# Optimization experiments

Hardware: AMD Instinct MI355X
Metric: run time of the kernel (lower is better)

Reference implementation:

```python
import jax, jax.numpy as jnp
import numpy as np

P = 3          # graph partitions
CO = 64        # out_channels
KS = 9         # temporal kernel size (Gamma)
STRIDE = 1     # temporal stride
EPS = 1e-3     # keras BatchNormalization default epsilon


def setup_inputs() -> dict:
    key = jax.random.key(0)
    k1, k2, k3 = jax.random.split(key, 3)
    x = jax.random.normal(k1, (32, 64, 300, 25), dtype=jnp.float32)      # (N, C_in, L, V)
    A = jax.random.uniform(k2, (3, 25, 25), dtype=jnp.float32)           # (P, V, V)
    W = jax.random.normal(k3, (64, 192), dtype=jnp.float32) * 0.05       # (C_in, C_out*P)
    gamma = jnp.ones((64,), dtype=jnp.float32)
    beta = jnp.zeros((64,), dtype=jnp.float32)
    mean = jnp.zeros((64,), dtype=jnp.float32)
    var = jnp.ones((64,), dtype=jnp.float32)
    return {"x": x, "A": A, "W": W, "gamma": gamma, "beta": beta, "mean": mean, "var": var}


def _lt_matrix(L):
    # sum of shifted identities: lt[r, r + i*STRIDE] = 1 for i in [0, KS//STRIDE)
    lt = jnp.zeros((L, L), dtype=jnp.float32)
    for i in range(KS // STRIDE):
        lt = lt + jnp.eye(L, k=i * STRIDE, dtype=jnp.float32)
    return lt


def reference(x, A, W, gamma, beta, mean, var):
    N, C, L, V = x.shape
    res = x  # identity residual (in_channels == out_channels, stride == 1)
    # 1x1 conv: (N,C,L,V) x (C, CO*P) -> (N, CO*P, L, V); channel k = c*P + p (split into CO groups of P)
    y = jnp.einsum('nclv,ck->nklv', x, W)
    y = y.reshape(N, CO, P, L, V)  # (N, C_out, P, L, V)
    # partitioned graph matmul over joints: contract V with A[p]
    z = jnp.einsum('ncplv,pvw->ncplw', y, A)
    # temporal aggregation via handcrafted banded matrix, then sum over partitions
    lt = _lt_matrix(L)
    t = jnp.einsum('ncplv,lm->ncmv', z, lt)  # partition sum fused into einsum
    # BN (inference) over channel axis + ReLU
    inv = gamma / jnp.sqrt(var + EPS)
    xn = (t - mean[None, :, None, None]) * inv[None, :, None, None] + beta[None, :, None, None]
    xn = jax.nn.relu(xn)
    # residual add + final ReLU (dropout is identity at inference)
    return jax.nn.relu(xn + res)
```

## Files before the change

kernel.cpp:

```cpp
#include <hip/hip_runtime.h>
#include <cstdint>
#include <cstddef>

typedef short bf16x8 __attribute__((ext_vector_type(8)));
typedef float f32x4 __attribute__((ext_vector_type(4)));

#define EPS 1e-3f

__device__ __forceinline__ short f32_to_bf16s(float f) {
    union { float f; uint32_t u; } v; v.f = f;
    uint32_t u = v.u;
    return (short)((u + 0x7FFFu + ((u >> 16) & 1u)) >> 16);
}

__global__ __launch_bounds__(256) void prep_kernel(const float* __restrict__ A,
                                                   const float* __restrict__ W,
                                                   unsigned short* __restrict__ wt,
                                                   unsigned short* __restrict__ at) {
    int idx = blockIdx.x * 256 + threadIdx.x;
    if (idx < 12288) {
        int kp = idx >> 6, ci = idx & 63;
        wt[idx] = (unsigned short)f32_to_bf16s(W[ci * 192 + kp]);
    } else {
        int j = idx - 12288;
        if (j < 3072) {
            int w = j / 96, k = j - w * 96;
            float val = 0.f;
            if (w < 25 && k < 75) {
                int p = k / 25, v = k - p * 25;
                val = A[(p * 25 + v) * 25 + w];
            }
            at[j] = (unsigned short)f32_to_bf16s(val);
        }
    }
}

__global__ __launch_bounds__(512, 4) void mega_kernel(
    const float* __restrict__ x,
    const unsigned short* __restrict__ wt,
    const unsigned short* __restrict__ at,
    const float* __restrict__ gamma, const float* __restrict__ beta,
    const float* __restrict__ mean, const float* __restrict__ var,
    float* __restrict__ out) {
    int ch = blockIdx.x, n = blockIdx.y;
    int l0 = ch * 10;
    int tid = threadIdx.x;
    int wv = tid >> 6, lane = tid & 63, q = lane >> 4, lcol = lane & 15;

    __shared__ short smem[16640];
    __shared__ float scs[64], shs[64];

    if (tid < 64) {
        float sc = gamma[tid] * rsqrtf(var[tid] + EPS);
        scs[tid] = sc;
        shs[tid] = beta[tid] - mean[tid] * sc;
    }

    #pragma unroll 1
    for (int rep = 0; rep < 4; ++rep) {
        int cidx = tid + rep * 512;
        if (cidx < 1600) {
            int ci = cidx / 25, v = cidx - ci * 25;
            const float* xp = x + (size_t)(n * 64 + ci) * 7500 + v;
            float vals[18];
            #pragma unroll
            for (int i = 0; i < 18; ++i) {
                int l = l0 - 8 + i;
                vals[i] = (l >= 0) ? xp[l * 25] : 0.f;
            }
            float run = 0.f;
            #pragma unroll
            for (int i = 0; i < 8; ++i) run += vals[i];
            int base = (ci >> 3) * 2056 + (ci & 7);
            #pragma unroll
            for (int j = 0; j < 10; ++j) {
                run += vals[j + 8];
                smem[base + (j * 25 + v) * 8] = f32_to_bf16s(run);
                run -= vals[j];
            }
        }
    }
    __syncthreads();

    bf16x8 b1[2][2];
    #pragma unroll
    for (int nt = 0; nt < 2; ++nt)
        #pragma unroll
        for (int s = 0; s < 2; ++s) {
            int col = wv * 32 + nt * 16 + lcol;
            b1[nt][s] = *(const bf16x8*)&smem[(4 * s + q) * 2056 + col * 8];
        }
    bf16x8 b2[2][3];
    #pragma unroll
    for (int nt = 0; nt < 2; ++nt)
        #pragma unroll
        for (int s = 0; s < 3; ++s)
            b2[nt][s] = *(const bf16x8*)(at + (size_t)(nt * 16 + lcol) * 96 + 32 * s + 8 * q);
    __syncthreads();

    for (int i = tid; i < 5120; i += 512) {
        int r = i >> 5, jj = 72 + (i & 31);
        smem[r * 104 + jj] = 0;
    }

    for (int g = 0; g < 4; ++g) {
        f32x4 acc[3][2];
        #pragma unroll
        for (int mt = 0; mt < 3; ++mt)
            #pragma unroll
            for (int nt = 0; nt < 2; ++nt) acc[mt][nt] = (f32x4){0.f, 0.f, 0.f, 0.f};
        #pragma unroll
        for (int s = 0; s < 2; ++s)
            #pragma unroll
            for (int mt = 0; mt < 3; ++mt) {
                bf16x8 a1 = *(const bf16x8*)(wt + (size_t)(g * 48 + mt * 16 + lcol) * 64 + 32 * s + 8 * q);
                #pragma unroll
                for (int nt = 0; nt < 2; ++nt)
                    acc[mt][nt] = __builtin_amdgcn_mfma_f32_16x16x32_bf16(a1, b1[nt][s], acc[mt][nt], 0, 0, 0);
            }
        __syncthreads();
        #pragma unroll
        for (int mt = 0; mt < 3; ++mt)
            #pragma unroll
            for (int nt = 0; nt < 2; ++nt) {
                int col = wv * 32 + nt * 16 + lcol;
                if (col < 250) {
                    int ll = col / 25, v = col - ll * 25;
                    #pragma unroll
                    for (int r = 0; r < 4; ++r) {
                        int kp = mt * 16 + 4 * q + r;
                        int cl = kp / 3, p = kp - cl * 3;
                        smem[(ll * 16 + cl) * 104 + p * 25 + v] = f32_to_bf16s(acc[mt][nt][r]);
                    }
                }
            }
        __syncthreads();
        for (int l = wv; l < 10; l += 8) {
            f32x4 c0 = {0.f, 0.f, 0.f, 0.f}, c1 = {0.f, 0.f, 0.f, 0.f};
            #pragma unroll
            for (int s = 0; s < 3; ++s) {
                bf16x8 a2 = *(const bf16x8*)&smem[(l * 16 + lcol) * 104 + 32 * s + 8 * q];
                c0 = __builtin_amdgcn_mfma_f32_16x16x32_bf16(a2, b2[0][s], c0, 0, 0, 0);
                c1 = __builtin_amdgcn_mfma_f32_16x16x32_bf16(a2, b2[1][s], c1, 0, 0, 0);
            }
            #pragma unroll
            for (int nt = 0; nt < 2; ++nt) {
                int w = nt * 16 + lcol;
                if (w < 25) {
                    f32x4 cc = nt ? c1 : c0;
                    #pragma unroll
                    for (int r = 0; r < 4; ++r) {
                        int c = g * 16 + 4 * q + r;
                        size_t gi = ((size_t)(n * 64 + c) * 300 + (l0 + l)) * 25 + w;
                        float o = fmaxf(cc[r] * scs[c] + shs[c], 0.f);
                        out[gi] = fmaxf(o + x[gi], 0.f);
                    }
                }
            }
        }
    }
}

extern "C" void kernel_launch(void* const* d_in, const int* in_sizes, int n_in,
                              void* d_out, int out_size, void* d_ws, size_t ws_size,
                              hipStream_t stream) {
    const float* x     = (const float*)d_in[0];
    const float* A     = (const float*)d_in[1];
    const float* W     = (const float*)d_in[2];
    const float* gamma = (const float*)d_in[3];
    const float* beta  = (const float*)d_in[4];
    const float* mean  = (const float*)d_in[5];
    const float* var   = (const float*)d_in[6];
    float* out = (float*)d_out;

    char* ws = (char*)d_ws;
    unsigned short* wt = (unsigned short*)ws;
    unsigned short* at = (unsigned short*)(ws + 24576);

    prep_kernel<<<60, 256, 0, stream>>>(A, W, wt, at);
    mega_kernel<<<dim3(30, 32), 512, 0, stream>>>(x, wt, at, gamma, beta, mean, var, out);
}
```

Before: 167.4 us.

## Batch x loads, prefetch residual early, rebalance graph-MFMA tiles across all waves

```diff
diff --git a/kernel.cpp b/kernel.cpp
--- a/kernel.cpp
+++ b/kernel.cpp
@@ -56,27 +56,53 @@
         shs[tid] = beta[tid] - mean[tid] * sc;
     }
 
-    #pragma unroll 1
-    for (int rep = 0; rep < 4; ++rep) {
-        int cidx = tid + rep * 512;
-        if (cidx < 1600) {
+    {
+        float va[3][18];
+        #pragma unroll
+        for (int rep = 0; rep < 3; ++rep) {
+            int cidx = tid + rep * 512;
             int ci = cidx / 25, v = cidx - ci * 25;
             const float* xp = x + (size_t)(n * 64 + ci) * 7500 + v;
-            float vals[18];
             #pragma unroll
             for (int i = 0; i < 18; ++i) {
                 int l = l0 - 8 + i;
-                vals[i] = (l >= 0) ? xp[l * 25] : 0.f;
-            }
+                va[rep][i] = (l >= 0) ? xp[l * 25] : 0.f;
+            }
+        }
+        #pragma unroll
+        for (int rep = 0; rep < 3; ++rep) {
+            int cidx = tid + rep * 512;
+            int ci = cidx / 25, v = cidx - ci * 25;
             float run = 0.f;
             #pragma unroll
-            for (int i = 0; i < 8; ++i) run += vals[i];
+            for (int i = 0; i < 8; ++i) run += va[rep][i];
             int base = (ci >> 3) * 2056 + (ci & 7);
             #pragma unroll
             for (int j = 0; j < 10; ++j) {
-                run += vals[j + 8];
+                run += va[rep][j + 8];
                 smem[base + (j * 25 + v) * 8] = f32_to_bf16s(run);
-                run -= vals[j];
+                run -= va[rep][j];
+            }
+        }
+        if (tid < 64) {
+            int cidx = 1536 + tid;
+            int ci = cidx / 25, v = cidx - ci * 25;
+            const float* xp = x + (size_t)(n * 64 + ci) * 7500 + v;
+            float vt[18];
+            #pragma unroll
+            for (int i = 0; i < 18; ++i) {
+                int l = l0 - 8 + i;
+                vt[i] = (l >= 0) ? xp[l * 25] : 0.f;
+            }
+            float run = 0.f;
+            #pragma unroll
+            for (int i = 0; i < 8; ++i) run += vt[i];
+            int base = (ci >> 3) * 2056 + (ci & 7);
+            #pragma unroll
+            for (int j = 0; j < 10; ++j) {
+                run += vt[j + 8];
+                smem[base + (j * 25 + v) * 8] = f32_to_bf16s(run);
+                run -= vt[j];
             }
         }
     }
@@ -118,6 +144,23 @@
                 for (int nt = 0; nt < 2; ++nt)
                     acc[mt][nt] = __builtin_amdgcn_mfma_f32_16x16x32_bf16(a1, b1[nt][s], acc[mt][nt], 0, 0, 0);
             }
+
+        float xres[3][4];
+        size_t gbase[3];
+        #pragma unroll
+        for (int t = 0; t < 3; ++t) {
+            int j = wv + 8 * t;
+            int l = j >> 1, nt = j & 1;
+            int w = nt * 16 + lcol;
+            bool valid = (j < 20) && (w < 25);
+            int c0 = g * 16 + 4 * q;
+            size_t gi0 = ((size_t)(n * 64 + c0) * 300 + (l0 + l)) * 25 + w;
+            gbase[t] = gi0;
+            #pragma unroll
+            for (int r = 0; r < 4; ++r)
+                xres[t][r] = valid ? x[gi0 + (size_t)r * 7500] : 0.f;
+        }
+
         __syncthreads();
         #pragma unroll
         for (int mt = 0; mt < 3; ++mt)
@@ -135,25 +178,26 @@
                 }
             }
         __syncthreads();
-        for (int l = wv; l < 10; l += 8) {
-            f32x4 c0 = {0.f, 0.f, 0.f, 0.f}, c1 = {0.f, 0.f, 0.f, 0.f};
-            #pragma unroll
-            for (int s = 0; s < 3; ++s) {
-                bf16x8 a2 = *(const bf16x8*)&smem[(l * 16 + lcol) * 104 + 32 * s + 8 * q];
-                c0 = __builtin_amdgcn_mfma_f32_16x16x32_bf16(a2, b2[0][s], c0, 0, 0, 0);
-                c1 = __builtin_amdgcn_mfma_f32_16x16x32_bf16(a2, b2[1][s], c1, 0, 0, 0);
-            }
-            #pragma unroll
-            for (int nt = 0; nt < 2; ++nt) {
+
+        #pragma unroll
+        for (int t = 0; t < 3; ++t) {
+            int j = wv + 8 * t;
+            if (j < 20) {
+                int l = j >> 1, nt = j & 1;
                 int w = nt * 16 + lcol;
+                f32x4 cacc = {0.f, 0.f, 0.f, 0.f};
+                #pragma unroll
+                for (int s = 0; s < 3; ++s) {
+                    bf16x8 a2 = *(const bf16x8*)&smem[(l * 16 + lcol) * 104 + 32 * s + 8 * q];
+                    cacc = __builtin_amdgcn_mfma_f32_16x16x32_bf16(a2, b2[nt][s], cacc, 0, 0, 0);
+                }
                 if (w < 25) {
-                    f32x4 cc = nt ? c1 : c0;
                     #pragma unroll
                     for (int r = 0; r < 4; ++r) {
                         int c = g * 16 + 4 * q + r;
-                        size_t gi = ((size_t)(n * 64 + c) * 300 + (l0 + l)) * 25 + w;
-                        float o = fmaxf(cc[r] * scs[c] + shs[c], 0.f);
-                        out[gi] = fmaxf(o + x[gi], 0.f);
+                        float o = fmaxf(cacc[r] * scs[c] + shs[c], 0.f);
+                        float res = fmaxf(o + xres[t][r], 0.f);
+                        __builtin_nontemporal_store(res, &out[gbase[t] + (size_t)r * 7500]);
                     }
                 }
             }
```

New measurement: 172.6 us. 3.1% more time.

## Stage x tile in LDS with float4 loads and reuse it for residual

Applied to the files above, without the earlier changes.

```diff
diff --git a/kernel.cpp b/kernel.cpp
--- a/kernel.cpp
+++ b/kernel.cpp
@@ -9,8 +9,11 @@
 
 __device__ __forceinline__ short f32_to_bf16s(float f) {
     union { float f; uint32_t u; } v; v.f = f;
-    uint32_t u = v.u;
-    return (short)((u + 0x7FFFu + ((u >> 16) & 1u)) >> 16);
+    return (short)((v.u + 0x7FFFu + ((v.u >> 16) & 1u)) >> 16);
+}
+__device__ __forceinline__ float bf16s_to_f32(short s) {
+    union { uint32_t u; float f; } v; v.u = ((uint32_t)(unsigned short)s) << 16;
+    return v.f;
 }
 
 __global__ __launch_bounds__(256) void prep_kernel(const float* __restrict__ A,
@@ -42,107 +45,179 @@
     const float* __restrict__ gamma, const float* __restrict__ beta,
     const float* __restrict__ mean, const float* __restrict__ var,
     float* __restrict__ out) {
-    int ch = blockIdx.x, n = blockIdx.y;
-    int l0 = ch * 10;
-    int tid = threadIdx.x;
-    int wv = tid >> 6, lane = tid & 63, q = lane >> 4, lcol = lane & 15;
-
-    __shared__ short smem[16640];
+    const int ch = blockIdx.x, n = blockIdx.y;
+    const int l0 = ch * 8;
+    const int tid = threadIdx.x;
+    const int wv = tid >> 6, lane = tid & 63, q = lane >> 4, lcol = lane & 15;
+
+    __shared__ __align__(16) short R0[13312];
+    __shared__ __align__(16) short XsB[13312];
     __shared__ float scs[64], shs[64];
 
+    bf16x8 b2[2][3];
+    #pragma unroll
+    for (int nt = 0; nt < 2; ++nt)
+        #pragma unroll
+        for (int s = 0; s < 3; ++s)
+            b2[nt][s] = *(const bf16x8*)(at + (size_t)(nt * 16 + lcol) * 96 + 32 * s + 8 * q);
     if (tid < 64) {
         float sc = gamma[tid] * rsqrtf(var[tid] + EPS);
         scs[tid] = sc;
         shs[tid] = beta[tid] - mean[tid] * sc;
     }
 
+    {
+        const float* xn = x + (size_t)n * 480000;
+        const int e0 = l0 * 25 - 200;
+        #pragma unroll
+        for (int rep = 0; rep < 13; ++rep) {
+            int i = tid + rep * 512;
+            if (i < 6400) {
+                int ci = i / 100, j = i - ci * 100;
+                int eg = e0 + 4 * j;
+                float4 val = make_float4(0.f, 0.f, 0.f, 0.f);
+                if (eg >= 0 && eg <= 7496)
+                    val = *(const float4*)(xn + (size_t)ci * 7500 + eg);
+                short4 sv;
+                sv.x = f32_to_bf16s(val.x); sv.y = f32_to_bf16s(val.y);
+                sv.z = f32_to_bf16s(val.z); sv.w = f32_to_bf16s(val.w);
+                if (j < 50) *(short4*)&R0[ci * 208 + 4 * j] = sv;
+                else        *(short4*)&XsB[ci * 208 + 4 * (j - 50)] = sv;
+            }
+        }
+    }
+    __syncthreads();
+
+    float hv[4][8];
+    #pragma unroll
+    for (int rep = 0; rep < 3; ++rep) {
+        int col = tid + rep * 512;
+        int ci = col / 25, v = col - ci * 25;
+        const short* hp = &R0[ci * 208 + v];
+        #pragma unroll
+        for (int m = 0; m < 8; ++m) hv[rep][m] = bf16s_to_f32(hp[m * 25]);
+    }
+    if (tid < 64) {
+        int col = 1536 + tid;
+        int ci = col / 25, v = col - ci * 25;
+        const short* hp = &R0[ci * 208 + v];
+        #pragma unroll
+        for (int m = 0; m < 8; ++m) hv[3][m] = bf16s_to_f32(hp[m * 25]);
+    }
+    __syncthreads();
+
+    #pragma unroll
+    for (int rep = 0; rep < 4; ++rep) {
+        int col = (rep < 3) ? (tid + rep * 512) : (1536 + tid);
+        bool act = (rep < 3) || (tid < 64);
+        if (act) {
+            int ci = col / 25, v = col - ci * 25;
+            const short* bp = &XsB[ci * 208 + v];
+            float bv[8];
+            #pragma unroll
+            for (int m = 0; m < 8; ++m) bv[m] = bf16s_to_f32(bp[m * 25]);
+            float run = hv[rep][0] + hv[rep][1] + hv[rep][2] + hv[rep][3]
+                      + hv[rep][4] + hv[rep][5] + hv[rep][6] + hv[rep][7];
+            short* wb = &R0[(ci >> 3) * 1656 + (ci & 7)];
+            #pragma unroll
+            for (int j = 0; j < 8; ++j) {
+                run += bv[j];
+                wb[(j * 25 + v) * 8] = f32_to_bf16s(run);
+                if (j < 7) run -= hv[rep][j];
+            }
+        }
+    }
+    __syncthreads();
+
+    bf16x8 b1[2][2];
+    #pragma unroll
+    for (int i = 0; i < 2; ++i) {
+        int t = 8 * i + wv;
+        int colb = 16 * t + lcol;
+        if (colb > 207) colb = 207;
+        #pragma unroll
+        for (int s = 0; s < 2; ++s)
+            b1[i][s] = *(const bf16x8*)&R0[(4 * s + q) * 1656 + colb * 8];
+    }
+    bf16x8 a1[3][2];
+    #pragma unroll
+    for (int mt = 0; mt < 3; ++mt)
+        #pragma unroll
+        for (int s = 0; s < 2; ++s)
+            a1[mt][s] = *(const bf16x8*)(wt + (size_t)(mt * 16 + lcol) * 64 + 32 * s + 8 * q);
+    __syncthreads();
+
+    #pragma unroll
+    for (int i = tid; i < 2688; i += 512) {
+        int r = i / 21, kk = 75 + (i - r * 21);
+        R0[r * 104 + kk] = 0;
+    }
+
     #pragma unroll 1
-    for (int rep = 0; rep < 4; ++rep) {
-        int cidx = tid + rep * 512;
-        if (cidx < 1600) {
-            int ci = cidx / 25, v = cidx - ci * 25;
-            const float* xp = x + (size_t)(n * 64 + ci) * 7500 + v;
-            float vals[18];
-            #pragma unroll
-            for (int i = 0; i < 18; ++i) {
-                int l = l0 - 8 + i;
-                vals[i] = (l >= 0) ? xp[l * 25] : 0.f;
-            }
-            float run = 0.f;
-            #pragma unroll
-            for (int i = 0; i < 8; ++i) run += vals[i];
-            int base = (ci >> 3) * 2056 + (ci & 7);
-            #pragma unroll
-            for (int j = 0; j < 10; ++j) {
-                run += vals[j + 8];
-                smem[base + (j * 25 + v) * 8] = f32_to_bf16s(run);
-                run -= vals[j];
-            }
-        }
-    }
-    __syncthreads();
-
-    bf16x8 b1[2][2];
-    #pragma unroll
-    for (int nt = 0; nt < 2; ++nt)
-        #pragma unroll
-        for (int s = 0; s < 2; ++s) {
-            int col = wv * 32 + nt * 16 + lcol;
-            b1[nt][s] = *(const bf16x8*)&smem[(4 * s + q) * 2056 + col * 8];
-        }
-    bf16x8 b2[2][3];
-    #pragma unroll
-    for (int nt = 0; nt < 2; ++nt)
-        #pragma unroll
-        for (int s = 0; s < 3; ++s)
-            b2[nt][s] = *(const bf16x8*)(at + (size_t)(nt * 16 + lcol) * 96 + 32 * s + 8 * q);
-    __syncthreads();
-
-    for (int i = tid; i < 5120; i += 512) {
-        int r = i >> 5, jj = 72 + (i & 31);
-        smem[r * 104 + jj] = 0;
-    }
-
     for (int g = 0; g < 4; ++g) {
         f32x4 acc[3][2];
         #pragma unroll
         for (int mt = 0; mt < 3; ++mt)
             #pragma unroll
-            for (int nt = 0; nt < 2; ++nt) acc[mt][nt] = (f32x4){0.f, 0.f, 0.f, 0.f};
+            for (int i = 0; i < 2; ++i) acc[mt][i] = (f32x4){0.f, 0.f, 0.f, 0.f};
         #pragma unroll
         for (int s = 0; s < 2; ++s)
             #pragma unroll
             for (int mt = 0; mt < 3; ++mt) {
-                bf16x8 a1 = *(const bf16x8*)(wt + (size_t)(g * 48 + mt * 16 + lcol) * 64 + 32 * s + 8 * q);
+                bf16x8 av = a1[mt][s];
                 #pragma unroll
-                for (int nt = 0; nt < 2; ++nt)
-                    acc[mt][nt] = __builtin_amdgcn_mfma_f32_16x16x32_bf16(a1, b1[nt][s], acc[mt][nt], 0, 0, 0);
-            }
+                for (int i = 0; i < 2; ++i)
+                    acc[mt][i] = __builtin_amdgcn_mfma_f32_16x16x32_bf16(av, b1[i][s], acc[mt][i], 0, 0, 0);
+            }
+        {
+            int gn = (g < 3) ? g + 1 : 3;
+            #pragma unroll
+            for (int mt = 0; mt < 3; ++mt)
+                #pragma unroll
+                for (int s = 0; s < 2; ++s)
+                    a1[mt][s] = *(const bf16x8*)(wt + (size_t)(gn * 48 + mt * 16 + lcol) * 64 + 32 * s + 8 * q);
+        }
         __syncthreads();
         #pragma unroll
         for (int mt = 0; mt < 3; ++mt)
             #pragma unroll
-            for (int nt = 0; nt < 2; ++nt) {
-                int col = wv * 32 + nt * 16 + lcol;
-                if (col < 250) {
+            for (int i = 0; i < 2; ++i) {
+                int t = 8 * i + wv;
+                int col = 16 * t + lcol;
+                if (col < 200) {
                     int ll = col / 25, v = col - ll * 25;
                     #pragma unroll
                     for (int r = 0; r < 4; ++r) {
                         int kp = mt * 16 + 4 * q + r;
                         int cl = kp / 3, p = kp - cl * 3;
-                        smem[(ll * 16 + cl) * 104 + p * 25 + v] = f32_to_bf16s(acc[mt][nt][r]);
+                        R0[(ll * 16 + cl) * 104 + 25 * p + v] = f32_to_bf16s(acc[mt][i][r]);
                     }
                 }
             }
         __syncthreads();
-        for (int l = wv; l < 10; l += 8) {
-            f32x4 c0 = {0.f, 0.f, 0.f, 0.f}, c1 = {0.f, 0.f, 0.f, 0.f};
-            #pragma unroll
-            for (int s = 0; s < 3; ++s) {
-                bf16x8 a2 = *(const bf16x8*)&smem[(l * 16 + lcol) * 104 + 32 * s + 8 * q];
-                c0 = __builtin_amdgcn_mfma_f32_16x16x32_bf16(a2, b2[0][s], c0, 0, 0, 0);
-                c1 = __builtin_amdgcn_mfma_f32_16x16x32_bf16(a2, b2[1][s], c1, 0, 0, 0);
-            }
+
+        const int l = wv;
+        float res[2][4];
+        #pragma unroll
+        for (int nt = 0; nt < 2; ++nt) {
+            int w = nt * 16 + lcol;
+            int wr = (w < 25) ? w : 24;
+            #pragma unroll
+            for (int r = 0; r < 4; ++r)
+                res[nt][r] = bf16s_to_f32(XsB[(g * 16 + 4 * q + r) * 208 + l * 25 + wr]);
+        }
+        bf16x8 a2[3];
+        #pragma unroll
+        for (int s = 0; s < 3; ++s)
+            a2[s] = *(const bf16x8*)&R0[(l * 16 + lcol) * 104 + 32 * s + 8 * q];
+        f32x4 c0 = {0.f, 0.f, 0.f, 0.f}, c1 = {0.f, 0.f, 0.f, 0.f};
+        #pragma unroll
+        for (int s = 0; s < 3; ++s) {
+            c0 = __builtin_amdgcn_mfma_f32_16x16x32_bf16(a2[s], b2[0][s], c0, 0, 0, 0);
+            c1 = __builtin_amdgcn_mfma_f32_16x16x32_bf16(a2[s], b2[1][s], c1, 0, 0, 0);
+        }
+        int lg = l0 + l;
+        if (lg < 300) {
             #pragma unroll
             for (int nt = 0; nt < 2; ++nt) {
                 int w = nt * 16 + lcol;
@@ -151,9 +226,8 @@
                     #pragma unroll
                     for (int r = 0; r < 4; ++r) {
                         int c = g * 16 + 4 * q + r;
-                        size_t gi = ((size_t)(n * 64 + c) * 300 + (l0 + l)) * 25 + w;
                         float o = fmaxf(cc[r] * scs[c] + shs[c], 0.f);
-                        out[gi] = fmaxf(o + x[gi], 0.f);
+                        out[((size_t)(n * 64 + c) * 300 + lg) * 25 + w] = fmaxf(o + res[nt][r], 0.f);
                     }
                 }
             }
@@ -178,5 +252,5 @@
     unsigned short* at = (unsigned short*)(ws + 24576);
 
     prep_kernel<<<60, 256, 0, stream>>>(A, W, wt, at);
-    mega_kernel<<<dim3(30, 32), 512, 0, stream>>>(x, wt, at, gamma, beta, mean, var, out);
-}
+    mega_kernel<<<dim3(38, 32), 512, 0, stream>>>(x, wt, at, gamma, beta, mean, var, out);
+}
```

Result: slower. 182.4 us (+9.0%).

## Give each wave its own time step, removing block barriers in the channel loop

Applied to the files above, without the earlier changes.

```diff
diff --git a/kernel.cpp b/kernel.cpp
--- a/kernel.cpp
+++ b/kernel.cpp
@@ -9,8 +9,7 @@
 
 __device__ __forceinline__ short f32_to_bf16s(float f) {
     union { float f; uint32_t u; } v; v.f = f;
-    uint32_t u = v.u;
-    return (short)((u + 0x7FFFu + ((u >> 16) & 1u)) >> 16);
+    return (short)((v.u + 0x7FFFu + ((v.u >> 16) & 1u)) >> 16);
 }
 
 __global__ __launch_bounds__(256) void prep_kernel(const float* __restrict__ A,
@@ -42,18 +41,31 @@
     const float* __restrict__ gamma, const float* __restrict__ beta,
     const float* __restrict__ mean, const float* __restrict__ var,
     float* __restrict__ out) {
-    int ch = blockIdx.x, n = blockIdx.y;
-    int l0 = ch * 10;
-    int tid = threadIdx.x;
-    int wv = tid >> 6, lane = tid & 63, q = lane >> 4, lcol = lane & 15;
-
-    __shared__ short smem[16640];
+    const int ch = blockIdx.x, n = blockIdx.y;
+    const int l0 = ch * 8;
+    const int tid = threadIdx.x;
+    const int wv = tid >> 6, lane = tid & 63, q = lane >> 4, lcol = lane & 15;
+
+    __shared__ __align__(16) short xwL[13248];
+    __shared__ __align__(16) short Ys[13312];
     __shared__ float scs[64], shs[64];
 
+    bf16x8 b2[2][3];
+    #pragma unroll
+    for (int nt = 0; nt < 2; ++nt)
+        #pragma unroll
+        for (int s = 0; s < 3; ++s)
+            b2[nt][s] = *(const bf16x8*)(at + (size_t)(nt * 16 + lcol) * 96 + 32 * s + 8 * q);
     if (tid < 64) {
         float sc = gamma[tid] * rsqrtf(var[tid] + EPS);
         scs[tid] = sc;
         shs[tid] = beta[tid] - mean[tid] * sc;
+    }
+
+    #pragma unroll
+    for (int i = lane; i < 512; i += 64) {
+        int r = i >> 5, cc = 72 + (i & 31);
+        Ys[(wv * 16 + r) * 104 + cc] = 0;
     }
 
     #pragma unroll 1
@@ -62,20 +74,19 @@
         if (cidx < 1600) {
             int ci = cidx / 25, v = cidx - ci * 25;
             const float* xp = x + (size_t)(n * 64 + ci) * 7500 + v;
-            float vals[18];
-            #pragma unroll
-            for (int i = 0; i < 18; ++i) {
+            float vals[16];
+            #pragma unroll
+            for (int i = 0; i < 16; ++i) {
                 int l = l0 - 8 + i;
-                vals[i] = (l >= 0) ? xp[l * 25] : 0.f;
-            }
-            float run = 0.f;
-            #pragma unroll
-            for (int i = 0; i < 8; ++i) run += vals[i];
-            int base = (ci >> 3) * 2056 + (ci & 7);
-            #pragma unroll
-            for (int j = 0; j < 10; ++j) {
+                vals[i] = (l >= 0 && l < 300) ? xp[l * 25] : 0.f;
+            }
+            float run = vals[0] + vals[1] + vals[2] + vals[3]
+                      + vals[4] + vals[5] + vals[6] + vals[7];
+            short* wb = &xwL[(ci >> 3) * 1656 + (ci & 7)];
+            #pragma unroll
+            for (int j = 0; j < 8; ++j) {
                 run += vals[j + 8];
-                smem[base + (j * 25 + v) * 8] = f32_to_bf16s(run);
+                wb[(j * 25 + v) * 8] = f32_to_bf16s(run);
                 run -= vals[j];
             }
         }
@@ -84,26 +95,25 @@
 
     bf16x8 b1[2][2];
     #pragma unroll
-    for (int nt = 0; nt < 2; ++nt)
-        #pragma unroll
-        for (int s = 0; s < 2; ++s) {
-            int col = wv * 32 + nt * 16 + lcol;
-            b1[nt][s] = *(const bf16x8*)&smem[(4 * s + q) * 2056 + col * 8];
-        }
-    bf16x8 b2[2][3];
-    #pragma unroll
-    for (int nt = 0; nt < 2; ++nt)
-        #pragma unroll
-        for (int s = 0; s < 3; ++s)
-            b2[nt][s] = *(const bf16x8*)(at + (size_t)(nt * 16 + lcol) * 96 + 32 * s + 8 * q);
-    __syncthreads();
-
-    for (int i = tid; i < 5120; i += 512) {
-        int r = i >> 5, jj = 72 + (i & 31);
-        smem[r * 104 + jj] = 0;
-    }
-
+    for (int nt = 0; nt < 2; ++nt) {
+        int col = wv * 25 + nt * 16 + lcol;
+        #pragma unroll
+        for (int s = 0; s < 2; ++s)
+            b1[nt][s] = *(const bf16x8*)&xwL[(4 * s + q) * 1656 + col * 8];
+    }
+
+    const int lg = l0 + wv;
+    const size_t outrow = ((size_t)n * 64 * 300 + lg) * 25;
+
+    #pragma unroll 1
     for (int g = 0; g < 4; ++g) {
+        bf16x8 a1[3][2];
+        #pragma unroll
+        for (int mt = 0; mt < 3; ++mt)
+            #pragma unroll
+            for (int s = 0; s < 2; ++s)
+                a1[mt][s] = *(const bf16x8*)(wt + (size_t)(g * 48 + mt * 16 + lcol) * 64 + 32 * s + 8 * q);
+
         f32x4 acc[3][2];
         #pragma unroll
         for (int mt = 0; mt < 3; ++mt)
@@ -113,36 +123,48 @@
         for (int s = 0; s < 2; ++s)
             #pragma unroll
             for (int mt = 0; mt < 3; ++mt) {
-                bf16x8 a1 = *(const bf16x8*)(wt + (size_t)(g * 48 + mt * 16 + lcol) * 64 + 32 * s + 8 * q);
+                bf16x8 av = a1[mt][s];
                 #pragma unroll
                 for (int nt = 0; nt < 2; ++nt)
-                    acc[mt][nt] = __builtin_amdgcn_mfma_f32_16x16x32_bf16(a1, b1[nt][s], acc[mt][nt], 0, 0, 0);
-            }
-        __syncthreads();
+                    acc[mt][nt] = __builtin_amdgcn_mfma_f32_16x16x32_bf16(av, b1[nt][s], acc[mt][nt], 0, 0, 0);
+            }
+
+        float res[2][4];
+        #pragma unroll
+        for (int nt = 0; nt < 2; ++nt) {
+            int w = nt * 16 + lcol;
+            bool val = (w < 25) && (lg < 300);
+            #pragma unroll
+            for (int r = 0; r < 4; ++r) {
+                int c = g * 16 + 4 * q + r;
+                res[nt][r] = val ? x[outrow + (size_t)c * 7500 + w] : 0.f;
+            }
+        }
+
         #pragma unroll
         for (int mt = 0; mt < 3; ++mt)
             #pragma unroll
             for (int nt = 0; nt < 2; ++nt) {
-                int col = wv * 32 + nt * 16 + lcol;
-                if (col < 250) {
-                    int ll = col / 25, v = col - ll * 25;
+                int v = nt * 16 + lcol;
+                if (v < 25) {
                     #pragma unroll
                     for (int r = 0; r < 4; ++r) {
-                        int kp = mt * 16 + 4 * q + r;
-                        int cl = kp / 3, p = kp - cl * 3;
-                        smem[(ll * 16 + cl) * 104 + p * 25 + v] = f32_to_bf16s(acc[mt][nt][r]);
+                        int kpl = mt * 16 + 4 * q + r;
+                        int cl = kpl / 3, p = kpl - 3 * cl;
+                        Ys[(wv * 16 + cl) * 104 + 25 * p + v] = f32_to_bf16s(acc[mt][nt][r]);
                     }
                 }
             }
-        __syncthreads();
-        for (int l = wv; l < 10; l += 8) {
-            f32x4 c0 = {0.f, 0.f, 0.f, 0.f}, c1 = {0.f, 0.f, 0.f, 0.f};
-            #pragma unroll
-            for (int s = 0; s < 3; ++s) {
-                bf16x8 a2 = *(const bf16x8*)&smem[(l * 16 + lcol) * 104 + 32 * s + 8 * q];
-                c0 = __builtin_amdgcn_mfma_f32_16x16x32_bf16(a2, b2[0][s], c0, 0, 0, 0);
-                c1 = __builtin_amdgcn_mfma_f32_16x16x32_bf16(a2, b2[1][s], c1, 0, 0, 0);
-            }
+
+        f32x4 c0 = {0.f, 0.f, 0.f, 0.f}, c1 = {0.f, 0.f, 0.f, 0.f};
+        #pragma unroll
+        for (int s = 0; s < 3; ++s) {
+            bf16x8 a2 = *(const bf16x8*)&Ys[(wv * 16 + lcol) * 104 + 32 * s + 8 * q];
+            c0 = __builtin_amdgcn_mfma_f32_16x16x32_bf16(a2, b2[0][s], c0, 0, 0, 0);
+            c1 = __builtin_amdgcn_mfma_f32_16x16x32_bf16(a2, b2[1][s], c1, 0, 0, 0);
+        }
+
+        if (lg < 300) {
             #pragma unroll
             for (int nt = 0; nt < 2; ++nt) {
                 int w = nt * 16 + lcol;
@@ -151,9 +173,8 @@
                     #pragma unroll
                     for (int r = 0; r < 4; ++r) {
                         int c = g * 16 + 4 * q + r;
-                        size_t gi = ((size_t)(n * 64 + c) * 300 + (l0 + l)) * 25 + w;
                         float o = fmaxf(cc[r] * scs[c] + shs[c], 0.f);
-                        out[gi] = fmaxf(o + x[gi], 0.f);
+                        out[outrow + (size_t)c * 7500 + w] = fmaxf(o + res[nt][r], 0.f);
                     }
                 }
             }
@@ -178,5 +199,5 @@
     unsigned short* at = (unsigned short*)(ws + 24576);
 
     prep_kernel<<<60, 256, 0, stream>>>(A, W, wt, at);
-    mega_kernel<<<dim3(30, 32), 512, 0, stream>>>(x, wt, at, gamma, beta, mean, var, out);
-}
+    mega_kernel<<<dim3(38, 32), 512, 0, stream>>>(x, wt, at, gamma, beta, mean, var, out);
+}
```

After: 165.1 us. About the same (-1.4%).
